# Kernel optimization log

Hardware: AMD Instinct MI355X
Metric: run time of the kernel (lower is better)

## Reference

```python
import jax, jax.numpy as jnp
import numpy as np

# Grid / filter configuration (matches init_kwargs)
NLAT_IN, NLON_IN = 361, 720
NLAT_OUT, NLON_OUT = 361, 720
K = 9                       # kernel_size for piecewise-linear basis, kernel_shape=[3,4]
PSCALE = NLON_IN // NLON_OUT  # longitude stride between output longitudes
NNZ = 65536
B, CIN, COUT = 2, 64, 64


def setup_inputs() -> dict:
    key = jax.random.key(0)
    k0, k1, k2, k3, k4, k5 = jax.random.split(key, 6)
    x = jax.random.normal(k0, (B, CIN, NLAT_IN, NLON_IN), dtype=jnp.float32)
    psi_ker_idx = jax.random.randint(k1, (NNZ,), 0, K)
    psi_row_idx = jax.random.randint(k2, (NNZ,), 0, NLAT_OUT)
    psi_col_idx = jax.random.randint(k3, (NNZ,), 0, NLAT_IN * NLON_IN)
    # quadrature-merged, normalized basis values are small positive numbers
    psi_vals = jax.random.uniform(k4, (NNZ,), dtype=jnp.float32) / K
    scale = (1.0 / (CIN * K)) ** 0.5
    weight = scale * jax.random.normal(k5, (COUT, CIN, K), dtype=jnp.float32)
    bias = jnp.zeros((COUT,), dtype=jnp.float32)
    return {
        "x": x,
        "psi_vals": psi_vals,
        "weight": weight,
        "bias": bias,
        "psi_ker_idx": psi_ker_idx,
        "psi_row_idx": psi_row_idx,
        "psi_col_idx": psi_col_idx,
    }


def reference(x, psi_vals, weight, bias, psi_ker_idx, psi_row_idx, psi_col_idx):
    """DISCO S2 conv: y[b,c,k,lo,p] = sum_nz psi_vals * x[b,c,lat_in, (lon_in+p*PSCALE)%NLON_IN]
    restricted to nz with ker==k, row==lo; then channel mixing with weight (COUT,CIN,K) + bias.
    Matches torch fallback which rolls x by PSCALE per output longitude and does sparse bmm."""
    b, c, nlat_in, nlon_in = x.shape
    lat_in = psi_col_idx // nlon_in          # (nnz,)
    lon_in = psi_col_idx % nlon_in           # (nnz,)
    seg = psi_ker_idx * NLAT_OUT + psi_row_idx  # (nnz,) segment id over (K, nlat_out)
    xf = x.reshape(b * c, nlat_in, nlon_in)

    def step(carry, p):
        lon = (lon_in + p * PSCALE) % nlon_in        # rolled longitude index, (nnz,)
        g = xf[:, lat_in, lon]                       # (BC, nnz) gather
        contrib = (psi_vals * g).T                   # (nnz, BC)
        yk = jax.ops.segment_sum(contrib, seg, num_segments=K * NLAT_OUT)  # (K*nlat_out, BC)
        y = yk.reshape(K, NLAT_OUT, b, c)
        o = jnp.einsum("klbc,ock->bol", y, weight)   # (B, COUT, nlat_out)
        return carry, o

    _, ys = jax.lax.scan(step, None, jnp.arange(NLON_OUT))  # (nlon_out, B, COUT, nlat_out)
    out = jnp.moveaxis(ys, 0, -1)                            # (B, COUT, nlat_out, nlon_out)
    return out + bias[None, :, None, None]
```

## Files before the change

### kernel.cpp

```cpp
#include <hip/hip_runtime.h>

typedef unsigned int uint;
typedef unsigned short ushort;

#define NLAT 361
#define NLON 720
#define NNZT 65536
#define CIN 64
#define COUT 64
#define NK 9
#define PADL 784
#define ROWCAP 384
#define CKTOT 576
#define YPS 168
#define WTS 640
#define XROWB (16*PADL*8)

typedef __attribute__((ext_vector_type(8))) short short8v;
typedef __attribute__((ext_vector_type(4))) float f32x4;

__device__ __forceinline__ float bfu(uint u){ return __uint_as_float(u<<16); }
__device__ __forceinline__ float bfh(uint u){ return __uint_as_float(u & 0xffff0000u); }
__device__ __forceinline__ ushort f2bf(float f){
  uint b = __float_as_uint(f);
  return (ushort)((b + 0x7fffu + ((b>>16)&1u)) >> 16);
}
__device__ __forceinline__ uint packbf2(float f0, float f1){
  uint b0 = __float_as_uint(f0), b1 = __float_as_uint(f1);
  uint r0 = (b0 + 0x7fffu + ((b0>>16)&1u)) >> 16;
  uint r1 = ((b1 + 0x7fffu + ((b1>>16)&1u)) >> 16) << 16;
  return r0 | r1;
}

__global__ __launch_bounds__(256) void k_csr(const int* __restrict__ ker, const int* __restrict__ row,
                                             const int* __restrict__ col, const float* __restrict__ vals,
                                             int2* __restrict__ meta_g, int* __restrict__ kptr_g){
  const int lo = blockIdx.x, tid = threadIdx.x;
  __shared__ int cnt2[256*NK];
  #pragma unroll
  for (int kk=0;kk<NK;kk++) cnt2[tid*NK+kk]=0;
  __syncthreads();
  for (int i=tid;i<NNZT;i+=256) if (row[i]==lo) cnt2[tid*NK + ker[i]]++;
  __syncthreads();
  if (tid==0){
    int run=0;
    for (int kk=0;kk<NK;kk++){
      kptr_g[lo*10+kk]=run;
      for (int t=0;t<256;t++){ int tmp=cnt2[t*NK+kk]; cnt2[t*NK+kk]=run; run+=tmp; }
    }
    kptr_g[lo*10+9]=run;
  }
  __syncthreads();
  for (int i=tid;i<NNZT;i+=256) if (row[i]==lo){
    int kk=ker[i];
    int off=cnt2[tid*NK+kk]++;
    if (off<ROWCAP){
      int c=col[i];
      int lat=c/NLON, lon=c-lat*NLON;
      uint vb = __float_as_uint(vals[i]) & 0xfffffc00u;
      meta_g[lo*ROWCAP+off]=make_int2(lat*XROWB + lon*8, (int)(vb | (uint)lon));
    }
  }
}

__global__ __launch_bounds__(256) void k_xb(const float* __restrict__ x, ushort* __restrict__ xb){
  const int bid=blockIdx.x, tid=threadIdx.x;
  const int b=bid/NLAT, lat=bid-b*NLAT;
  const float* xs = x + (size_t)b*CIN*NLAT*NLON + (size_t)lat*NLON;
  ushort* xd = xb + (size_t)(b*NLAT+lat)*16*PADL*4;
  const size_t S=(size_t)NLAT*NLON;
  for (int idx=tid; idx<16*PADL; idx+=256){
    int cq=idx/PADL, j=idx-cq*PADL;
    int jj = (j<NLON)? j : j-NLON;
    const float* xc = xs + (size_t)(cq*4)*S + jj;
    uint lo32 = packbf2(xc[0], xc[S]);
    uint hi32 = packbf2(xc[2*S], xc[3*S]);
    *(uint2*)(xd + (size_t)(cq*PADL + j)*4) = make_uint2(lo32, hi32);
  }
}

__global__ __launch_bounds__(256) void k_wt(const float* __restrict__ w, ushort* __restrict__ wt){
  int idx = blockIdx.x*256 + threadIdx.x;
  if (idx >= COUT*WTS) return;
  int oc = idx/WTS, ckl = idx-oc*WTS;
  int chunk = ckl/160, q = ckl-chunk*160;
  ushort v = 0;
  if (q < 144){
    int wvq=q/36, r=q-wvq*36;
    int kk=r>>2, j=r&3;
    v = f2bf(w[oc*CKTOT + (chunk*16 + wvq*4 + j)*NK + kk]);
  }
  wt[oc*WTS + ckl] = v;
}

template<int USE_XB>
__global__ __launch_bounds__(256,4) void k_main(const float* __restrict__ x, const ushort* __restrict__ xb,
    const int2* __restrict__ meta_g, const int* __restrict__ kptr_g,
    const ushort* __restrict__ wt, const float* __restrict__ bias, float* __restrict__ out){
  const int nwg = NLAT*6;
  const int qq = nwg/8, rr = nwg%8;
  const int xcd = blockIdx.x & 7, sidx = blockIdx.x >> 3;
  const int bid = (xcd<rr ? xcd*(qq+1) : rr*(qq+1) + (xcd-rr)*qq) + sidx;
  const int tid=threadIdx.x;
  const int lo=bid/6; const int rem=bid-lo*6;
  const int b=rem/3, pq=rem-(rem/3)*3;

  __shared__ int2 meta[ROWCAP];
  __shared__ __align__(16) ushort Yp[64*YPS];

  int kp[10];
  #pragma unroll
  for (int kk=0;kk<10;kk++){ int v=kptr_g[lo*10+kk]; kp[kk]=v<ROWCAP?v:ROWCAP; }
  for (int i=tid;i<kp[9];i+=256) meta[i]=meta_g[lo*ROWCAP+i];
  for (int idx=tid; idx<64*8; idx+=256){
    int p=idx>>3, j=idx&7;
    *(uint*)((char*)Yp + p*(YPS*2) + 288 + j*4) = 0;
  }
  __syncthreads();

  const int lane=tid&63, wv=tid>>6;
  const int wvu = __builtin_amdgcn_readfirstlane(wv);
  const int l15=lane&15, kg=lane>>4;
  const char* xb8 = (const char*)xb + (size_t)b*NLAT*(size_t)XROWB;
  const char* wtb = (const char*)wt + ((wv*16+l15)*WTS + kg*8)*2;
  const char* ypb = (const char*)Yp + l15*(YPS*2) + kg*16;
  char* ydst = (char*)Yp + lane*(YPS*2) + wv*72;

#define GADDR(M) ((uint)(M).x + lanep8 + (((((uint)(M).y)&0x3ffu) >= thr) ? (uint)-5760 : 0u))
#define GVAL(M)  __uint_as_float(((uint)(M).y) & 0xfffffc00u)
#define GCONS(U,V,ACC,AI) { ACC[0][AI]+=(V)*bfu((U).x); ACC[1][AI]+=(V)*bfh((U).x); \
                            ACC[2][AI]+=(V)*bfu((U).y); ACC[3][AI]+=(V)*bfh((U).y); }
#define GB1F(M,ACC,AI) { \
      uint lon=((uint)(M).y)&0x3ffu; float v=GVAL(M); \
      int lat=(int)(((uint)(M).x)/(uint)XROWB); \
      int s=(int)lon+p0; s=(s>=NLON)?s-NLON:s; \
      int widx=s+lane; widx=(widx>=NLON)?widx-NLON:widx; \
      int base=((b*CIN + chunk*16 + wv*4)*NLAT + lat)*NLON + widx; \
      ACC[0][AI]+=v*x[base]; ACC[1][AI]+=v*x[base+NLAT*NLON]; \
      ACC[2][AI]+=v*x[base+2*NLAT*NLON]; ACC[3][AI]+=v*x[base+3*NLAT*NLON]; }

#define GSEG(ACC,KI,AI) { \
      int i=kp[KI]; const int e=kp[(KI)+1]; \
      if (USE_XB){ \
        for (; i+7<e; i+=8){ \
          int2 m0=meta[i],m1=meta[i+1],m2=meta[i+2],m3=meta[i+3]; \
          int2 m4=meta[i+4],m5=meta[i+5],m6=meta[i+6],m7=meta[i+7]; \
          uint2 u0=*(const uint2*)(xbase+GADDR(m0)); uint2 u1=*(const uint2*)(xbase+GADDR(m1)); \
          uint2 u2=*(const uint2*)(xbase+GADDR(m2)); uint2 u3=*(const uint2*)(xbase+GADDR(m3)); \
          uint2 u4=*(const uint2*)(xbase+GADDR(m4)); uint2 u5=*(const uint2*)(xbase+GADDR(m5)); \
          uint2 u6=*(const uint2*)(xbase+GADDR(m6)); uint2 u7=*(const uint2*)(xbase+GADDR(m7)); \
          GCONS(u0,GVAL(m0),ACC,AI); GCONS(u1,GVAL(m1),ACC,AI); \
          GCONS(u2,GVAL(m2),ACC,AI); GCONS(u3,GVAL(m3),ACC,AI); \
          GCONS(u4,GVAL(m4),ACC,AI); GCONS(u5,GVAL(m5),ACC,AI); \
          GCONS(u6,GVAL(m6),ACC,AI); GCONS(u7,GVAL(m7),ACC,AI); \
        } \
        for (; i+3<e; i+=4){ \
          int2 m0=meta[i],m1=meta[i+1],m2=meta[i+2],m3=meta[i+3]; \
          uint2 u0=*(const uint2*)(xbase+GADDR(m0)); uint2 u1=*(const uint2*)(xbase+GADDR(m1)); \
          uint2 u2=*(const uint2*)(xbase+GADDR(m2)); uint2 u3=*(const uint2*)(xbase+GADDR(m3)); \
          GCONS(u0,GVAL(m0),ACC,AI); GCONS(u1,GVAL(m1),ACC,AI); \
          GCONS(u2,GVAL(m2),ACC,AI); GCONS(u3,GVAL(m3),ACC,AI); \
        } \
        for (; i<e; i++){ int2 m0=meta[i]; \
          uint2 u0=*(const uint2*)(xbase+GADDR(m0)); GCONS(u0,GVAL(m0),ACC,AI); } \
      } else { \
        for (; i<e; i++){ int2 m0=meta[i]; GB1F(m0,ACC,AI); } \
      } }

  f32x4 outacc[4][4];
  #pragma unroll
  for (int a=0;a<4;a++)
    #pragma unroll
    for (int c2=0;c2<4;c2++) outacc[a][c2]=(f32x4)0.f;

  for (int chunk=0;chunk<4;chunk++){
    const char* xbase = xb8 + (size_t)(chunk*4+wvu)*(PADL*8);
    #pragma unroll
    for (int pt=0;pt<4;pt++){
      const int p0 = pq*240 + pt*64;
      const uint thr = (uint)(NLON - p0);
      const uint lanep8 = (uint)(lane + p0)*8u;
      const bool act = (pt<3) || (lane<48);

      {
        float acc1[4][5];
        #pragma unroll
        for (int j=0;j<4;j++)
          #pragma unroll
          for (int kk=0;kk<5;kk++) acc1[j][kk]=0.f;
        if (act){ GSEG(acc1,0,0) GSEG(acc1,1,1) GSEG(acc1,2,2) GSEG(acc1,3,3) GSEG(acc1,4,4) }
        __syncthreads();
        if (act){
          #pragma unroll
          for (int kk=0;kk<5;kk++){
            *(uint*)(ydst + (kk*4+0)*2) = packbf2(acc1[0][kk], acc1[1][kk]);
            *(uint*)(ydst + (kk*4+2)*2) = packbf2(acc1[2][kk], acc1[3][kk]);
          }
        }
      }
      {
        float acc2[4][4];
        #pragma unroll
        for (int j=0;j<4;j++)
          #pragma unroll
          for (int kk=0;kk<4;kk++) acc2[j][kk]=0.f;
        if (act){
          GSEG(acc2,5,0) GSEG(acc2,6,1) GSEG(acc2,7,2) GSEG(acc2,8,3)
          #pragma unroll
          for (int kk=0;kk<4;kk++){
            *(uint*)(ydst + ((kk+5)*4+0)*2) = packbf2(acc2[0][kk], acc2[1][kk]);
            *(uint*)(ydst + ((kk+5)*4+2)*2) = packbf2(acc2[2][kk], acc2[3][kk]);
          }
        }
      }
      __syncthreads();
      #pragma unroll
      for (int ptile=0;ptile<4;ptile++){
        #pragma unroll
        for (int ks=0;ks<5;ks++){
          short8v bf = *(const short8v*)(ypb + ptile*(16*YPS*2) + ks*64);
          short8v afk = *(const short8v*)(wtb + (chunk*160 + ks*32)*2);
          outacc[pt][ptile] = __builtin_amdgcn_mfma_f32_16x16x32_bf16(afk, bf, outacc[pt][ptile], 0, 0, 0);
        }
      }
    }
  }
  #pragma unroll
  for (int pt=0;pt<4;pt++)
    #pragma unroll
    for (int ptile=0;ptile<4;ptile++){
      const int pidx = pt*64 + ptile*16;
      if (pidx < 240){
        #pragma unroll
        for (int r=0;r<4;r++){
          int oc = wv*16 + kg*4 + r;
          int p  = pq*240 + pidx + l15;
          out[((size_t)(b*COUT+oc)*NLAT + lo)*NLON + p] = outacc[pt][ptile][r] + bias[oc];
        }
      }
    }
}

extern "C" void kernel_launch(void* const* d_in, const int* in_sizes, int n_in,
                              void* d_out, int out_size, void* d_ws, size_t ws_size,
                              hipStream_t stream){
  const float* x   =(const float*)d_in[0];
  const float* vals=(const float*)d_in[1];
  const float* w   =(const float*)d_in[2];
  const float* bias=(const float*)d_in[3];
  const int* ker=(const int*)d_in[4];
  const int* row=(const int*)d_in[5];
  const int* col=(const int*)d_in[6];
  float* out=(float*)d_out;

  const size_t META_B=(size_t)NLAT*ROWCAP*sizeof(int2);
  const size_t KPTR_B=((size_t)NLAT*10*sizeof(int)+15)&~(size_t)15;
  const size_t WT_B=((size_t)COUT*WTS*sizeof(ushort)+15)&~(size_t)15;
  const size_t XB_B=(size_t)2*NLAT*16*PADL*4*sizeof(ushort);
  int2* meta_g=(int2*)d_ws;
  int*  kptr_g=(int*)((char*)d_ws+META_B);
  ushort* wt=(ushort*)((char*)d_ws+META_B+KPTR_B);
  ushort* xb=(ushort*)((char*)d_ws+META_B+KPTR_B+WT_B);
  const bool use_xb = ws_size >= META_B+KPTR_B+WT_B+XB_B;

  k_csr<<<dim3(NLAT), dim3(256), 0, stream>>>(ker,row,col,vals,meta_g,kptr_g);
  k_wt <<<dim3((COUT*WTS+255)/256), dim3(256), 0, stream>>>(w, wt);
  if (use_xb){
    k_xb<<<dim3(2*NLAT), dim3(256), 0, stream>>>(x, xb);
    k_main<1><<<dim3(NLAT*6), dim3(256), 0, stream>>>(x,xb,meta_g,kptr_g,wt,bias,out);
  } else {
    k_main<0><<<dim3(NLAT*6), dim3(256), 0, stream>>>(x,xb,meta_g,kptr_g,wt,bias,out);
  }
}
```

Before: 2.127 ms.

## Use cooperative grid-synced lockstep schedule and sort CSR entries by address

The main kernel now runs one workgroup per (lat_out, batch) on a 722-block grid instead of 2166. Each block loops over all three longitude thirds, and a grid-wide sync each (pt, chunk) step keeps all blocks in lockstep so their gathers from the bf16 x copy share L2 working sets. The CSR build kernel sorts each row's nonzeros by (kernel index, address) with an O(n^2) rank sort, so consecutive gathers hit nearby memory. This adds grid-sync overhead, reduces parallelism per block, and makes the preprocessing kernel more expensive.

```diff
diff --git a/kernel.cpp b/kernel.cpp
--- a/kernel.cpp
+++ b/kernel.cpp
@@ -1,7 +1,9 @@
 #include <hip/hip_runtime.h>
+#include <hip/hip_cooperative_groups.h>
 
 typedef unsigned int uint;
 typedef unsigned short ushort;
+typedef unsigned char uchar;
 
 #define NLAT 361
 #define NLON 720
@@ -15,6 +17,7 @@
 #define YPS 168
 #define WTS 640
 #define XROWB (16*PADL*8)
+#define GRIDC 722
 
 typedef __attribute__((ext_vector_type(8))) short short8v;
 typedef __attribute__((ext_vector_type(4))) float f32x4;
@@ -36,30 +39,44 @@
                                              const int* __restrict__ col, const float* __restrict__ vals,
                                              int2* __restrict__ meta_g, int* __restrict__ kptr_g){
   const int lo = blockIdx.x, tid = threadIdx.x;
-  __shared__ int cnt2[256*NK];
-  #pragma unroll
-  for (int kk=0;kk<NK;kk++) cnt2[tid*NK+kk]=0;
+  __shared__ int cnt[256];
+  __shared__ int2 list[ROWCAP];
+  __shared__ uchar kl[ROWCAP];
+  __shared__ int kc[NK];
+  __shared__ int ntot;
+  int c=0;
+  for (int i=tid;i<NNZT;i+=256) if (row[i]==lo) c++;
+  cnt[tid]=c;
+  if (tid<NK) kc[tid]=0;
   __syncthreads();
-  for (int i=tid;i<NNZT;i+=256) if (row[i]==lo) cnt2[tid*NK + ker[i]]++;
+  if (tid==0){ int run=0; for (int t=0;t<256;t++){ int tmp=cnt[t]; cnt[t]=run; run+=tmp; } ntot=run; }
   __syncthreads();
+  int off=cnt[tid];
+  for (int i=tid;i<NNZT;i+=256) if (row[i]==lo){
+    if (off<ROWCAP){
+      int cc=col[i]; int lat=cc/NLON, lon=cc-lat*NLON;
+      uint vb=__float_as_uint(vals[i])&0xfffffc00u;
+      list[off]=make_int2(lat*XROWB+lon*8, (int)(vb|(uint)lon));
+      kl[off]=(uchar)ker[i];
+      atomicAdd(&kc[ker[i]],1);
+    }
+    off++;
+  }
+  __syncthreads();
+  int n = ntot; if (n>ROWCAP) n=ROWCAP;
+  for (int i=tid;i<n;i+=256){
+    uint ki = ((uint)kl[i]<<23) | ((uint)list[i].x>>3);
+    int r=0;
+    for (int j=0;j<n;j++){
+      uint kj = ((uint)kl[j]<<23) | ((uint)list[j].x>>3);
+      r += (kj<ki) || (kj==ki && j<i);
+    }
+    meta_g[lo*ROWCAP+r]=list[i];
+  }
   if (tid==0){
     int run=0;
-    for (int kk=0;kk<NK;kk++){
-      kptr_g[lo*10+kk]=run;
-      for (int t=0;t<256;t++){ int tmp=cnt2[t*NK+kk]; cnt2[t*NK+kk]=run; run+=tmp; }
-    }
-    kptr_g[lo*10+9]=run;
-  }
-  __syncthreads();
-  for (int i=tid;i<NNZT;i+=256) if (row[i]==lo){
-    int kk=ker[i];
-    int off=cnt2[tid*NK+kk]++;
-    if (off<ROWCAP){
-      int c=col[i];
-      int lat=c/NLON, lon=c-lat*NLON;
-      uint vb = __float_as_uint(vals[i]) & 0xfffffc00u;
-      meta_g[lo*ROWCAP+off]=make_int2(lat*XROWB + lon*8, (int)(vb | (uint)lon));
-    }
+    for (int k=0;k<NK;k++){ kptr_g[lo*10+k]=run; run+=kc[k]; }
+    kptr_g[lo*10+9]=n;
   }
 }
 
@@ -93,17 +110,13 @@
   wt[oc*WTS + ckl] = v;
 }
 
-template<int USE_XB>
-__global__ __launch_bounds__(256,4) void k_main(const float* __restrict__ x, const ushort* __restrict__ xb,
+template<int USE_XB, int SYNC>
+__global__ __launch_bounds__(256,4) void k_coop(const float* __restrict__ x, const ushort* __restrict__ xb,
     const int2* __restrict__ meta_g, const int* __restrict__ kptr_g,
     const ushort* __restrict__ wt, const float* __restrict__ bias, float* __restrict__ out){
-  const int nwg = NLAT*6;
-  const int qq = nwg/8, rr = nwg%8;
-  const int xcd = blockIdx.x & 7, sidx = blockIdx.x >> 3;
-  const int bid = (xcd<rr ? xcd*(qq+1) : rr*(qq+1) + (xcd-rr)*qq) + sidx;
-  const int tid=threadIdx.x;
-  const int lo=bid/6; const int rem=bid-lo*6;
-  const int b=rem/3, pq=rem-(rem/3)*3;
+  const int wid=blockIdx.x, tid=threadIdx.x;
+  const int lane=tid&63, wv=tid>>6, l15=lane&15, kg=lane>>4;
+  const int lo=wid>>1, b=wid&1;
 
   __shared__ int2 meta[ROWCAP];
   __shared__ __align__(16) ushort Yp[64*YPS];
@@ -114,13 +127,11 @@
   for (int i=tid;i<kp[9];i+=256) meta[i]=meta_g[lo*ROWCAP+i];
   for (int idx=tid; idx<64*8; idx+=256){
     int p=idx>>3, j=idx&7;
-    *(uint*)((char*)Yp + p*(YPS*2) + 288 + j*4) = 0;
+    *(uint*)((char*)Yp + p*(YPS*2) + 288 + j*4)=0;
   }
   __syncthreads();
 
-  const int lane=tid&63, wv=tid>>6;
   const int wvu = __builtin_amdgcn_readfirstlane(wv);
-  const int l15=lane&15, kg=lane>>4;
   const char* xb8 = (const char*)xb + (size_t)b*NLAT*(size_t)XROWB;
   const char* wtb = (const char*)wt + ((wv*16+l15)*WTS + kg*8)*2;
   const char* ypb = (const char*)Yp + l15*(YPS*2) + kg*16;
@@ -135,9 +146,9 @@
       int lat=(int)(((uint)(M).x)/(uint)XROWB); \
       int s=(int)lon+p0; s=(s>=NLON)?s-NLON:s; \
       int widx=s+lane; widx=(widx>=NLON)?widx-NLON:widx; \
-      int base=((b*CIN + chunk*16 + wv*4)*NLAT + lat)*NLON + widx; \
-      ACC[0][AI]+=v*x[base]; ACC[1][AI]+=v*x[base+NLAT*NLON]; \
-      ACC[2][AI]+=v*x[base+2*NLAT*NLON]; ACC[3][AI]+=v*x[base+3*NLAT*NLON]; }
+      int fb=((b*CIN + chunk*16 + wv*4)*NLAT + lat)*NLON + widx; \
+      ACC[0][AI]+=v*x[fb]; ACC[1][AI]+=v*x[fb+NLAT*NLON]; \
+      ACC[2][AI]+=v*x[fb+2*NLAT*NLON]; ACC[3][AI]+=v*x[fb+3*NLAT*NLON]; }
 
 #define GSEG(ACC,KI,AI) { \
       int i=kp[KI]; const int e=kp[(KI)+1]; \
@@ -167,78 +178,87 @@
         for (; i<e; i++){ int2 m0=meta[i]; GB1F(m0,ACC,AI); } \
       } }
 
-  f32x4 outacc[4][4];
+  f32x4 outacc[3][4];
   #pragma unroll
-  for (int a=0;a<4;a++)
+  for (int a=0;a<3;a++)
     #pragma unroll
     for (int c2=0;c2<4;c2++) outacc[a][c2]=(f32x4)0.f;
 
-  for (int chunk=0;chunk<4;chunk++){
-    const char* xbase = xb8 + (size_t)(chunk*4+wvu)*(PADL*8);
-    #pragma unroll
-    for (int pt=0;pt<4;pt++){
-      const int p0 = pq*240 + pt*64;
-      const uint thr = (uint)(NLON - p0);
-      const uint lanep8 = (uint)(lane + p0)*8u;
-      const bool act = (pt<3) || (lane<48);
-
-      {
-        float acc1[4][5];
+  for (int pt=0;pt<4;pt++){
+    for (int chunk=0;chunk<4;chunk++){
+      if constexpr (SYNC) cooperative_groups::this_grid().sync();
+      const char* xbase = xb8 + (size_t)(chunk*4+wvu)*(PADL*8);
+      for (int it=0;it<3;it++){
+        const int p0 = it*240 + pt*64;
+        const uint thr = (uint)(NLON-p0);
+        const uint lanep8 = (uint)(lane+p0)*8u;
+        const bool act = (pt<3) || (lane<48);
+
+        {
+          float acc1[4][5];
+          #pragma unroll
+          for (int j=0;j<4;j++)
+            #pragma unroll
+            for (int kk=0;kk<5;kk++) acc1[j][kk]=0.f;
+          if (act){ GSEG(acc1,0,0) GSEG(acc1,1,1) GSEG(acc1,2,2) GSEG(acc1,3,3) GSEG(acc1,4,4) }
+          __syncthreads();
+          if (act){
+            #pragma unroll
+            for (int kk=0;kk<5;kk++){
+              *(uint*)(ydst + (kk*4+0)*2) = packbf2(acc1[0][kk], acc1[1][kk]);
+              *(uint*)(ydst + (kk*4+2)*2) = packbf2(acc1[2][kk], acc1[3][kk]);
+            }
+          }
+        }
+        {
+          float acc2[4][4];
+          #pragma unroll
+          for (int j=0;j<4;j++)
+            #pragma unroll
+            for (int kk=0;kk<4;kk++) acc2[j][kk]=0.f;
+          if (act){
+            GSEG(acc2,5,0) GSEG(acc2,6,1) GSEG(acc2,7,2) GSEG(acc2,8,3)
+            #pragma unroll
+            for (int kk=0;kk<4;kk++){
+              *(uint*)(ydst + ((kk+5)*4+0)*2) = packbf2(acc2[0][kk], acc2[1][kk]);
+              *(uint*)(ydst + ((kk+5)*4+2)*2) = packbf2(acc2[2][kk], acc2[3][kk]);
+            }
+          }
+        }
+        __syncthreads();
         #pragma unroll
-        for (int j=0;j<4;j++)
+        for (int ptile=0;ptile<4;ptile++){
           #pragma unroll
-          for (int kk=0;kk<5;kk++) acc1[j][kk]=0.f;
-        if (act){ GSEG(acc1,0,0) GSEG(acc1,1,1) GSEG(acc1,2,2) GSEG(acc1,3,3) GSEG(acc1,4,4) }
-        __syncthreads();
-        if (act){
-          #pragma unroll
-          for (int kk=0;kk<5;kk++){
-            *(uint*)(ydst + (kk*4+0)*2) = packbf2(acc1[0][kk], acc1[1][kk]);
-            *(uint*)(ydst + (kk*4+2)*2) = packbf2(acc1[2][kk], acc1[3][kk]);
+          for (int ks=0;ks<5;ks++){
+            short8v bf = *(const short8v*)(ypb + ptile*(16*YPS*2) + ks*64);
+            short8v afk = *(const short8v*)(wtb + (chunk*160 + ks*32)*2);
+            outacc[it][ptile]=__builtin_amdgcn_mfma_f32_16x16x32_bf16(afk,bf,outacc[it][ptile],0,0,0);
           }
         }
       }
-      {
-        float acc2[4][4];
-        #pragma unroll
-        for (int j=0;j<4;j++)
+    }
+    #pragma unroll
+    for (int it=0;it<3;it++){
+      #pragma unroll
+      for (int ptile=0;ptile<4;ptile++){
+        const int pidx = pt*64 + ptile*16;
+        if (pidx < 240){
           #pragma unroll
-          for (int kk=0;kk<4;kk++) acc2[j][kk]=0.f;
-        if (act){
-          GSEG(acc2,5,0) GSEG(acc2,6,1) GSEG(acc2,7,2) GSEG(acc2,8,3)
-          #pragma unroll
-          for (int kk=0;kk<4;kk++){
-            *(uint*)(ydst + ((kk+5)*4+0)*2) = packbf2(acc2[0][kk], acc2[1][kk]);
-            *(uint*)(ydst + ((kk+5)*4+2)*2) = packbf2(acc2[2][kk], acc2[3][kk]);
+          for (int r=0;r<4;r++){
+            int oc = wv*16 + kg*4 + r;
+            out[((size_t)(b*COUT+oc)*NLAT + lo)*NLON + it*240 + pidx + l15]
+              = outacc[it][ptile][r] + bias[oc];
           }
         }
-      }
-      __syncthreads();
-      #pragma unroll
-      for (int ptile=0;ptile<4;ptile++){
-        #pragma unroll
-        for (int ks=0;ks<5;ks++){
-          short8v bf = *(const short8v*)(ypb + ptile*(16*YPS*2) + ks*64);
-          short8v afk = *(const short8v*)(wtb + (chunk*160 + ks*32)*2);
-          outacc[pt][ptile] = __builtin_amdgcn_mfma_f32_16x16x32_bf16(afk, bf, outacc[pt][ptile], 0, 0, 0);
-        }
+        outacc[it][ptile]=(f32x4)0.f;
       }
     }
   }
-  #pragma unroll
-  for (int pt=0;pt<4;pt++)
-    #pragma unroll
-    for (int ptile=0;ptile<4;ptile++){
-      const int pidx = pt*64 + ptile*16;
-      if (pidx < 240){
-        #pragma unroll
-        for (int r=0;r<4;r++){
-          int oc = wv*16 + kg*4 + r;
-          int p  = pq*240 + pidx + l15;
-          out[((size_t)(b*COUT+oc)*NLAT + lo)*NLON + p] = outacc[pt][ptile][r] + bias[oc];
-        }
-      }
-    }
+#undef GSEG
+#undef GB1F
+#undef GCONS
+#undef GVAL
+#undef GADDR
 }
 
 extern "C" void kernel_launch(void* const* d_in, const int* in_sizes, int n_in,
@@ -251,7 +271,7 @@
   const int* ker=(const int*)d_in[4];
   const int* row=(const int*)d_in[5];
   const int* col=(const int*)d_in[6];
-  float* out=(float*)d_out;
+  float* outp=(float*)d_out;
 
   const size_t META_B=(size_t)NLAT*ROWCAP*sizeof(int2);
   const size_t KPTR_B=((size_t)NLAT*10*sizeof(int)+15)&~(size_t)15;
@@ -265,10 +285,30 @@
 
   k_csr<<<dim3(NLAT), dim3(256), 0, stream>>>(ker,row,col,vals,meta_g,kptr_g);
   k_wt <<<dim3((COUT*WTS+255)/256), dim3(256), 0, stream>>>(w, wt);
-  if (use_xb){
+  if (use_xb)
     k_xb<<<dim3(2*NLAT), dim3(256), 0, stream>>>(x, xb);
-    k_main<1><<<dim3(NLAT*6), dim3(256), 0, stream>>>(x,xb,meta_g,kptr_g,wt,bias,out);
-  } else {
-    k_main<0><<<dim3(NLAT*6), dim3(256), 0, stream>>>(x,xb,meta_g,kptr_g,wt,bias,out);
-  }
-}
+
+  int dev=0; (void)hipGetDevice(&dev);
+  int coopAttr=0; (void)hipDeviceGetAttribute(&coopAttr, hipDeviceAttributeCooperativeLaunch, dev);
+  int ncu=0; (void)hipDeviceGetAttribute(&ncu, hipDeviceAttributeMultiprocessorCount, dev);
+
+  typedef void (*KFn)(const float*, const ushort*, const int2*, const int*,
+                      const ushort*, const float*, float*);
+  KFn fsync = use_xb ? (KFn)&k_coop<1,1> : (KFn)&k_coop<0,1>;
+  int nb=0;
+  (void)hipOccupancyMaxActiveBlocksPerMultiprocessor(&nb, fsync, 256, 0);
+
+  bool coop = (coopAttr!=0) && ((long)nb*(long)ncu >= (long)GRIDC);
+  if (coop){
+    const ushort* xbc = xb; const ushort* wtc = wt;
+    const int2* mgc = meta_g; const int* kpc = kptr_g;
+    void* params[7] = {(void*)&x,(void*)&xbc,(void*)&mgc,(void*)&kpc,(void*)&wtc,(void*)&bias,(void*)&outp};
+    hipError_t e = hipLaunchCooperativeKernel(reinterpret_cast<const void*>(fsync),
+                                              dim3(GRIDC), dim3(256), params, 0, stream);
+    if (e != hipSuccess){ (void)hipGetLastError(); coop=false; }
+  }
+  if (!coop){
+    if (use_xb) k_coop<1,0><<<dim3(GRIDC), dim3(256), 0, stream>>>(x,xb,meta_g,kptr_g,wt,bias,outp);
+    else        k_coop<0,0><<<dim3(GRIDC), dim3(256), 0, stream>>>(x,xb,meta_g,kptr_g,wt,bias,outp);
+  }
+}
```

Result: faster. 2.063 ms (-3.0%).
